# Kernel tuning notes

Measured on AMD Instinct MI355X. Metric: run time of the kernel, lower is better.

The kernel has to match this reference:

```python
import jax, jax.numpy as jnp
import numpy as np

B, S, D, H = 4, 1024, 768, 12
Dh = D // H
EPS = 1e-5


def _layer_norm(x, g, b):
    mu = jnp.mean(x, axis=-1, keepdims=True)
    var = jnp.var(x, axis=-1, keepdims=True)
    return (x - mu) * jax.lax.rsqrt(var + EPS) * g + b


def _mha(q_in, k_in, v_in, Wq, Wk, Wv, Wo, bias):
    # Wq/Wk/Wv: [H, D, Dh] (per-head projections, batched over heads)
    q = jnp.einsum('bsd,hdk->bhsk', q_in, Wq)
    k = jnp.einsum('btd,hdk->bhtk', k_in, Wk)
    v = jnp.einsum('btd,hdk->bhtk', v_in, Wv)
    w = jnp.einsum('bhsk,bhtk->bhst', q, k) * (Dh ** -0.5)
    a = jax.nn.softmax(w + bias, axis=-1)  # bias: 0 / -inf additive mask
    o = jnp.einsum('bhst,bhtk->bhsk', a, v)
    o = o.transpose(0, 2, 1, 3).reshape(q_in.shape[0], q_in.shape[1], H * Dh)  # concat heads
    return o @ Wo


def setup_inputs():
    key = jax.random.key(0)
    ks = jax.random.split(key, 16)
    s = 0.02
    inp = {
        'key_enc': jax.random.normal(ks[0], (B, S, D), jnp.float32),
        'value_enc': jax.random.normal(ks[1], (B, S, D), jnp.float32),
        'x': jax.random.normal(ks[2], (B, S, D), jnp.float32),
        'src_mask': jnp.ones((B, S), jnp.int32),
        'tgt_mask': jnp.ones((B, S), jnp.int32),
        'Wq_m': jax.random.normal(ks[3], (H, D, Dh), jnp.float32) * s,
        'Wk_m': jax.random.normal(ks[4], (H, D, Dh), jnp.float32) * s,
        'Wv_m': jax.random.normal(ks[5], (H, D, Dh), jnp.float32) * s,
        'Wo_m': jax.random.normal(ks[6], (D, D), jnp.float32) * s,
        'Wq_c': jax.random.normal(ks[7], (H, D, Dh), jnp.float32) * s,
        'Wk_c': jax.random.normal(ks[8], (H, D, Dh), jnp.float32) * s,
        'Wv_c': jax.random.normal(ks[9], (H, D, Dh), jnp.float32) * s,
        'Wo_c': jax.random.normal(ks[10], (D, D), jnp.float32) * s,
        'ln1_g': jnp.ones((D,), jnp.float32), 'ln1_b': jnp.zeros((D,), jnp.float32),
        'ln2_g': jnp.ones((D,), jnp.float32), 'ln2_b': jnp.zeros((D,), jnp.float32),
        'ln3_g': jnp.ones((D,), jnp.float32), 'ln3_b': jnp.zeros((D,), jnp.float32),
        'W1': jax.random.normal(ks[11], (D, 4 * D), jnp.float32) * s,
        'b1': jnp.zeros((4 * D,), jnp.float32),
        'W2': jax.random.normal(ks[12], (4 * D, D), jnp.float32) * s,
        'b2': jnp.zeros((D,), jnp.float32),
    }
    return inp


def reference(key_enc, value_enc, x, src_mask, tgt_mask,
              Wq_m, Wk_m, Wv_m, Wo_m, Wq_c, Wk_c, Wv_c, Wo_c,
              ln1_g, ln1_b, ln2_g, ln2_b, ln3_g, ln3_b, W1, b1, W2, b2):
    neg_inf = jnp.float32(-jnp.inf)
    causal = jnp.tril(jnp.ones((S, S), bool))
    # masked self-attn: causal AND target padding mask (mask broadcasts over query rows)
    allow_m = causal[None, None, :, :] & (tgt_mask[:, None, None, :] != 0)
    bias_m = jnp.where(allow_m, jnp.float32(0.0), neg_inf)
    h = _layer_norm(x + _mha(x, x, x, Wq_m, Wk_m, Wv_m, Wo_m, bias_m), ln1_g, ln1_b)
    # cross-attn: keys from `key_enc`, values from `value_enc`, queries from decoder stream
    allow_c = (src_mask[:, None, None, :] != 0)
    bias_c = jnp.where(allow_c, jnp.float32(0.0), neg_inf)
    h = _layer_norm(h + _mha(h, key_enc, value_enc, Wq_c, Wk_c, Wv_c, Wo_c, bias_c), ln2_g, ln2_b)
    # MLP with exact (erf) GELU, as torch nn.GELU default
    mlp = jax.nn.gelu(h @ W1 + b1, approximate=False) @ W2 + b2
    return _layer_norm(h + mlp, ln3_g, ln3_b)
```

## Files before the change

kernel.cpp:

```cpp
#include <hip/hip_runtime.h>
#include <math.h>

#define BB 4
#define SS 1024
#define DD 768
#define HH 12
#define DHD 64
#define MROWS 4096
#define FF 3072
#define WPC (DD * DD)

typedef unsigned short u16;
typedef float f32x4 __attribute__((ext_vector_type(4)));
typedef __bf16 bf16x8 __attribute__((ext_vector_type(8)));
typedef unsigned short u16x8 __attribute__((ext_vector_type(8)));
typedef unsigned short u16x4 __attribute__((ext_vector_type(4)));

static __device__ __forceinline__ float bf2f(u16 u) {
    union { unsigned int i; float f; } c; c.i = ((unsigned int)u) << 16; return c.f;
}
static __device__ __forceinline__ u16 f2bf(float f) {
    return __builtin_bit_cast(u16, static_cast<__bf16>(f));
}
static __device__ __forceinline__ int xcd_swz(int total) {
    const int bid = (int)blockIdx.x;
    return (bid & 7) * (total >> 3) + (bid >> 3);
}

#define LDST 40

static __device__ __forceinline__ void gemm128_core(
    const u16* __restrict__ A, const u16* __restrict__ Bt,
    int K,
    const float* __restrict__ bias, int do_gelu,
    u16* __restrict__ Cbf, int ldcbf, int cboff,
    int row0, int col0, u16* As, u16* Bs)
{
    const int tid  = threadIdx.x;
    const int lane = tid & 63;
    const int w    = tid >> 6;
    const int wm = (w >> 1) * 64;
    const int wn = (w & 1) * 64;

    const int srow = tid >> 1;
    const int skc  = (tid & 1) * 16;

    const u16* Ap = A  + (size_t)(row0 + srow) * K + skc;
    const u16* Bp = Bt + (size_t)(col0 + srow) * K + skc;
    u16* AsW = &As[srow * LDST + skc];
    u16* BsW = &Bs[srow * LDST + skc];

    const int fr = lane & 15;
    const int fk = (lane >> 4) * 8;

    f32x4 acc[4][4] = {};

    u16x8 aa0, aa1, ba0, ba1;
    u16x8 ab0, ab1, bb0, bb1;
    aa0 = *(const u16x8*)(Ap);
    aa1 = *(const u16x8*)(Ap + 8);
    ba0 = *(const u16x8*)(Bp);
    ba1 = *(const u16x8*)(Bp + 8);
    ab0 = *(const u16x8*)(Ap + 32);
    ab1 = *(const u16x8*)(Ap + 40);
    bb0 = *(const u16x8*)(Bp + 32);
    bb1 = *(const u16x8*)(Bp + 40);

    for (int k0 = 0; k0 < K; k0 += 64) {
        if (k0) __syncthreads();
        *(u16x8*)(AsW)     = aa0;
        *(u16x8*)(AsW + 8) = aa1;
        *(u16x8*)(BsW)     = ba0;
        *(u16x8*)(BsW + 8) = ba1;
        __syncthreads();
        if (k0 + 64 < K) {
            aa0 = *(const u16x8*)(Ap + k0 + 64);
            aa1 = *(const u16x8*)(Ap + k0 + 72);
            ba0 = *(const u16x8*)(Bp + k0 + 64);
            ba1 = *(const u16x8*)(Bp + k0 + 72);
        }
        {
            bf16x8 af[4], bfv[4];
#pragma unroll
            for (int mi = 0; mi < 4; ++mi)
                af[mi] = __builtin_bit_cast(bf16x8,
                    *(const u16x8*)(&As[(wm + 16 * mi + fr) * LDST + fk]));
#pragma unroll
            for (int ni = 0; ni < 4; ++ni)
                bfv[ni] = __builtin_bit_cast(bf16x8,
                    *(const u16x8*)(&Bs[(wn + 16 * ni + fr) * LDST + fk]));
#pragma unroll
            for (int mi = 0; mi < 4; ++mi)
#pragma unroll
                for (int ni = 0; ni < 4; ++ni)
                    acc[mi][ni] = __builtin_amdgcn_mfma_f32_16x16x32_bf16(
                        af[mi], bfv[ni], acc[mi][ni], 0, 0, 0);
        }

        __syncthreads();
        *(u16x8*)(AsW)     = ab0;
        *(u16x8*)(AsW + 8) = ab1;
        *(u16x8*)(BsW)     = bb0;
        *(u16x8*)(BsW + 8) = bb1;
        __syncthreads();
        if (k0 + 96 < K) {
            ab0 = *(const u16x8*)(Ap + k0 + 96);
            ab1 = *(const u16x8*)(Ap + k0 + 104);
            bb0 = *(const u16x8*)(Bp + k0 + 96);
            bb1 = *(const u16x8*)(Bp + k0 + 104);
        }
        {
            bf16x8 af[4], bfv[4];
#pragma unroll
            for (int mi = 0; mi < 4; ++mi)
                af[mi] = __builtin_bit_cast(bf16x8,
                    *(const u16x8*)(&As[(wm + 16 * mi + fr) * LDST + fk]));
#pragma unroll
            for (int ni = 0; ni < 4; ++ni)
                bfv[ni] = __builtin_bit_cast(bf16x8,
                    *(const u16x8*)(&Bs[(wn + 16 * ni + fr) * LDST + fk]));
#pragma unroll
            for (int mi = 0; mi < 4; ++mi)
#pragma unroll
                for (int ni = 0; ni < 4; ++ni)
                    acc[mi][ni] = __builtin_amdgcn_mfma_f32_16x16x32_bf16(
                        af[mi], bfv[ni], acc[mi][ni], 0, 0, 0);
        }
    }

    const int orow0 = row0 + wm + (lane >> 4) * 4;
    const int ocol0 = col0 + wn + fr;
#pragma unroll
    for (int mi = 0; mi < 4; ++mi) {
#pragma unroll
        for (int ni = 0; ni < 4; ++ni) {
            const int col = ocol0 + ni * 16;
            const float bv = bias ? bias[col] : 0.0f;
#pragma unroll
            for (int r = 0; r < 4; ++r) {
                const int row = orow0 + mi * 16 + r;
                float v = acc[mi][ni][r] + bv;
                if (do_gelu) v = 0.5f * v * (1.0f + erff(v * 0.70710678118654752f));
                Cbf[(size_t)row * ldcbf + cboff + col] = f2bf(v);
            }
        }
    }
}

__global__ __launch_bounds__(256) void gemm128_mlp1(
    const u16* __restrict__ A, const u16* __restrict__ Bt,
    const float* __restrict__ bias, u16* __restrict__ Cbf)
{
    __shared__ u16 As[128 * LDST];
    __shared__ u16 Bs[128 * LDST];
    const int lid = xcd_swz(24 * 32);
    gemm128_core(A, Bt, DD, bias, 1, Cbf, FF, 0,
                 (lid / 24) * 128, (lid % 24) * 128, As, Bs);
}

__global__ __launch_bounds__(256) void gemm128_proj(
    const u16* __restrict__ BFx, const u16* __restrict__ BFK,
    const u16* __restrict__ BFV, const u16* __restrict__ Wm6,
    u16* __restrict__ QKV, u16* __restrict__ KVc)
{
    __shared__ u16 As[128 * LDST];
    __shared__ u16 Bs[128 * LDST];
    const int fid = xcd_swz(960);
    const u16* A; const u16* B; u16* C; int ldc, coff, row0, col0;
    if (fid < 576) {
        A = BFx; B = Wm6; C = QKV; ldc = 3 * DD; coff = 0;
        row0 = (fid / 18) * 128; col0 = (fid % 18) * 128;
    } else if (fid < 768) {
        const int l = fid - 576;
        A = BFK; B = Wm6 + 4 * WPC; C = KVc; ldc = 2 * DD; coff = 0;
        row0 = (l / 6) * 128; col0 = (l % 6) * 128;
    } else {
        const int l = fid - 768;
        A = BFV; B = Wm6 + 5 * WPC; C = KVc; ldc = 2 * DD; coff = DD;
        row0 = (l / 6) * 128; col0 = (l % 6) * 128;
    }
    gemm128_core(A, B, DD, nullptr, 0, C, ldc, coff, row0, col0, As, Bs);
}

static __device__ __forceinline__ void gemm64_core(
    const u16* __restrict__ A, const u16* __restrict__ Bt,
    int N, int Kstride, int Klen,
    const float* __restrict__ bias,
    const float* __restrict__ residf, const u16* __restrict__ residb,
    u16* __restrict__ Cbf, int ldcbf, int cboff,
    int row0, int col0, u16* As, u16* Bs)
{
    const int tid  = threadIdx.x;
    const int lane = tid & 63;
    const int w    = tid >> 6;
    const int wm = (w >> 1) * 32;
    const int wn = (w & 1) * 64;

    const int arow = tid >> 2;
    const int akc  = (tid & 3) * 8;
    const int brow = tid >> 1;
    const int bkc  = (tid & 1) * 16;

    const u16* Ap = A  + (size_t)(row0 + arow) * Kstride + akc;
    const u16* Bp = Bt + (size_t)(col0 + brow) * Kstride + bkc;
    u16* AsW = &As[arow * LDST + akc];
    u16* BsW = &Bs[brow * LDST + bkc];

    const int fr = lane & 15;
    const int fk = (lane >> 4) * 8;

    f32x4 acc[2][4] = {};

    u16x8 a0, b00, b01, a1, b10, b11;
    a0  = *(const u16x8*)(Ap);
    b00 = *(const u16x8*)(Bp);
    b01 = *(const u16x8*)(Bp + 8);
    a1  = *(const u16x8*)(Ap + 32);
    b10 = *(const u16x8*)(Bp + 32);
    b11 = *(const u16x8*)(Bp + 40);

    for (int k0 = 0; k0 < Klen; k0 += 64) {
        if (k0) __syncthreads();
        *(u16x8*)AsW       = a0;
        *(u16x8*)BsW       = b00;
        *(u16x8*)(BsW + 8) = b01;
        __syncthreads();
        if (k0 + 64 < Klen) {
            a0  = *(const u16x8*)(Ap + k0 + 64);
            b00 = *(const u16x8*)(Bp + k0 + 64);
            b01 = *(const u16x8*)(Bp + k0 + 72);
        }
        {
            bf16x8 af[2], bfv[4];
#pragma unroll
            for (int mi = 0; mi < 2; ++mi)
                af[mi] = __builtin_bit_cast(bf16x8,
                    *(const u16x8*)(&As[(wm + 16 * mi + fr) * LDST + fk]));
#pragma unroll
            for (int ni = 0; ni < 4; ++ni)
                bfv[ni] = __builtin_bit_cast(bf16x8,
                    *(const u16x8*)(&Bs[(wn + 16 * ni + fr) * LDST + fk]));
#pragma unroll
            for (int mi = 0; mi < 2; ++mi)
#pragma unroll
                for (int ni = 0; ni < 4; ++ni)
                    acc[mi][ni] = __builtin_amdgcn_mfma_f32_16x16x32_bf16(
                        af[mi], bfv[ni], acc[mi][ni], 0, 0, 0);
        }

        __syncthreads();
        *(u16x8*)AsW       = a1;
        *(u16x8*)BsW       = b10;
        *(u16x8*)(BsW + 8) = b11;
        __syncthreads();
        if (k0 + 96 < Klen) {
            a1  = *(const u16x8*)(Ap + k0 + 96);
            b10 = *(const u16x8*)(Bp + k0 + 96);
            b11 = *(const u16x8*)(Bp + k0 + 104);
        }
        {
            bf16x8 af[2], bfv[4];
#pragma unroll
            for (int mi = 0; mi < 2; ++mi)
                af[mi] = __builtin_bit_cast(bf16x8,
                    *(const u16x8*)(&As[(wm + 16 * mi + fr) * LDST + fk]));
#pragma unroll
            for (int ni = 0; ni < 4; ++ni)
                bfv[ni] = __builtin_bit_cast(bf16x8,
                    *(const u16x8*)(&Bs[(wn + 16 * ni + fr) * LDST + fk]));
#pragma unroll
            for (int mi = 0; mi < 2; ++mi)
#pragma unroll
                for (int ni = 0; ni < 4; ++ni)
                    acc[mi][ni] = __builtin_amdgcn_mfma_f32_16x16x32_bf16(
                        af[mi], bfv[ni], acc[mi][ni], 0, 0, 0);
        }
    }

    const int orow0 = row0 + wm + (lane >> 4) * 4;
    const int ocol0 = col0 + wn + fr;
#pragma unroll
    for (int mi = 0; mi < 2; ++mi) {
#pragma unroll
        for (int ni = 0; ni < 4; ++ni) {
            const int col = ocol0 + ni * 16;
            const float bv = bias ? bias[col] : 0.0f;
#pragma unroll
            for (int r = 0; r < 4; ++r) {
                const int row = orow0 + mi * 16 + r;
                float v = acc[mi][ni][r] + bv;
                if (residf) v += residf[(size_t)row * N + col];
                if (residb) v += bf2f(residb[(size_t)row * N + col]);
                Cbf[(size_t)row * ldcbf + cboff + col] = f2bf(v);
            }
        }
    }
}

__global__ __launch_bounds__(256) void gemm64(
    const u16* __restrict__ A, const u16* __restrict__ Bt, int K,
    const float* __restrict__ residf, const u16* __restrict__ residb,
    u16* __restrict__ Cbf, int ldcbf)
{
    __shared__ u16 As[64 * LDST];
    __shared__ u16 Bs[128 * LDST];
    const int lid = xcd_swz(6 * 64);
    gemm64_core(A, Bt, DD, K, K, nullptr, residf, residb, Cbf, ldcbf, 0,
                (lid / 6) * 64, (lid % 6) * 128, As, Bs);
}

__global__ __launch_bounds__(256) void gemm64_sk(
    const u16* __restrict__ A, const u16* __restrict__ Bt,
    u16* __restrict__ Cpair)
{
    __shared__ u16 As[64 * LDST];
    __shared__ u16 Bs[128 * LDST];
    const int lid = xcd_swz(6 * 64 * 2);
    const int x = lid % 6;
    const int rem = lid / 6;
    const int y = rem % 64;
    const int z = rem / 64;
    const int koff = z * (FF / 2);
    gemm64_core(A + koff, Bt + koff, DD, FF, FF / 2,
                nullptr, nullptr, nullptr,
                Cpair + (size_t)z * MROWS * DD, DD, 0,
                y * 64, x * 128, As, Bs);
}

static __device__ __forceinline__ void tcvt_body(
    const float* __restrict__ in, u16* __restrict__ out,
    int K, int N, int bx, int by)
{
    __shared__ float t[32][33];
    const int n0 = bx * 32, k0 = by * 32;
    const int tx = threadIdx.x & 31, ty = threadIdx.x >> 5;
#pragma unroll
    for (int j = 0; j < 4; ++j)
        t[ty + j * 8][tx] = in[(size_t)(k0 + ty + j * 8) * N + n0 + tx];
    __syncthreads();
#pragma unroll
    for (int j = 0; j < 4; ++j)
        out[(size_t)(n0 + ty + j * 8) * K + k0 + tx] = f2bf(t[tx][ty + j * 8]);
}

__global__ __launch_bounds__(256) void prep_all(
    const float* __restrict__ x, const float* __restrict__ key_enc,
    const float* __restrict__ value_enc,
    u16* __restrict__ BFx, u16* __restrict__ BFK, u16* __restrict__ BFV,
    const float* __restrict__ wq_m, const float* __restrict__ wk_m,
    const float* __restrict__ wv_m, const float* __restrict__ wq_c,
    const float* __restrict__ wk_c, const float* __restrict__ wv_c,
    u16* __restrict__ Wm6,
    const float* __restrict__ wom, const float* __restrict__ woc,
    const float* __restrict__ w1, const float* __restrict__ w2,
    u16* __restrict__ womt, u16* __restrict__ woct,
    u16* __restrict__ w1t, u16* __restrict__ w2t)
{
    const int fid = (int)blockIdx.x;
    const int tid = threadIdx.x;
    if (fid < 9216) {
        const int z = fid / 3072;
        const float* s = (z == 0) ? x : (z == 1) ? key_enc : value_enc;
        u16* d = (z == 0) ? BFx : (z == 1) ? BFK : BFV;
        const int i = (fid % 3072) * 256 + tid;
        float4 v = ((const float4*)s)[i];
        ushort4 o;
        o.x = f2bf(v.x); o.y = f2bf(v.y); o.z = f2bf(v.z); o.w = f2bf(v.w);
        ((ushort4*)d)[i] = o;
    } else if (fid < 12672) {
        const int l = fid - 9216;
        const int z = l / 48;
        const int r = l % 48;
        const int wi = z / 12, head = z % 12;
        const float* wsel = (wi == 0) ? wq_m : (wi == 1) ? wk_m :
                            (wi == 2) ? wv_m : (wi == 3) ? wq_c :
                            (wi == 4) ? wk_c : wv_c;
        const float* ib = wsel + (size_t)head * DD * DHD;
        u16* ob = Wm6 + (size_t)wi * WPC + (size_t)head * DHD * DD;
        __shared__ float t[32][33];
        const int n0 = (r % 2) * 32, k0 = (r / 2) * 32;
        const int tx = tid & 31, ty = tid >> 5;
#pragma unroll
        for (int j = 0; j < 4; ++j)
            t[ty + j * 8][tx] = ib[(size_t)(k0 + ty + j * 8) * DHD + n0 + tx];
        __syncthreads();
#pragma unroll
        for (int j = 0; j < 4; ++j)
            ob[(size_t)(n0 + ty + j * 8) * DD + k0 + tx] = f2bf(t[tx][ty + j * 8]);
    } else {
        const int l = fid - 12672;
        if (l < 576) {
            tcvt_body(wom, womt, DD, DD, l % 24, l / 24);
        } else if (l < 1152) {
            const int m = l - 576;
            tcvt_body(woc, woct, DD, DD, m % 24, m / 24);
        } else if (l < 3456) {
            const int m = l - 1152;
            tcvt_body(w1, w1t, DD, FF, m % 96, m / 96);
        } else {
            const int m = l - 3456;
            tcvt_body(w2, w2t, FF, DD, m % 24, m / 24);
        }
    }
}

#define KAST 72
#define PAST 136
#define CSC 0.18033688011112042f
__global__ __launch_bounds__(256) void attn_mfma_kernel(
    const u16* __restrict__ Q, int ldq,
    const u16* __restrict__ K, const u16* __restrict__ V, int ldkv,
    const int* __restrict__ kmask, u16* __restrict__ O, int causal)
{
    const int lid = xcd_swz(16 * BB * HH);
    const int qtl = lid % 16;
    const int bh  = lid / 16;
    const int qt = causal ? (15 - qtl) : qtl;
    const int b  = bh / HH;
    const int h  = bh % HH;
    const int tid  = threadIdx.x;
    const int lane = tid & 63;
    const int w    = tid >> 6;
    const int lr = lane & 15;
    const int lg = lane >> 4;

    __shared__ u16 Ks[128 * KAST];
    __shared__ u16 Ps[64 * PAST];
    __shared__ u16 Vt[64 * PAST];

    const int row0 = qt * 64;
    const int q0w  = row0 + w * 16;

    bf16x8 qf[2];
    {
        const u16* qp = Q + (size_t)(b * SS + q0w + lr) * ldq + h * DHD + lg * 8;
        qf[0] = __builtin_bit_cast(bf16x8, *(const u16x8*)(qp));
        qf[1] = __builtin_bit_cast(bf16x8, *(const u16x8*)(qp + 32));
    }

    const int sr  = tid >> 1;
    const int scb = (tid & 1) * 32;
    const int vk  = tid >> 1;
    const int vdb = (tid & 1) * 32;
    const int k6  = vk & 63;
    const int vcol = ((vk >> 6) << 6) | ((k6 & 15) << 2) | (k6 >> 4);

    f32x4 acc[4] = {};
    float lsum[4] = {0.0f, 0.0f, 0.0f, 0.0f};

    const int nkt = causal ? ((qt + 2) >> 1) : 8;

    u16x8 kr0, kr1, kr2, kr3, vr0, vr1, vr2, vr3;
    {
        const u16* kp = K + (size_t)(b * SS + sr) * ldkv + h * DHD + scb;
        kr0 = *(const u16x8*)(kp);
        kr1 = *(const u16x8*)(kp + 8);
        kr2 = *(const u16x8*)(kp + 16);
        kr3 = *(const u16x8*)(kp + 24);
        const u16* vp = V + (size_t)(b * SS + vk) * ldkv + h * DHD + vdb;
        vr0 = *(const u16x8*)(vp);
        vr1 = *(const u16x8*)(vp + 8);
        vr2 = *(const u16x8*)(vp + 16);
        vr3 = *(const u16x8*)(vp + 24);
    }

    for (int kt = 0; kt < nkt; ++kt) {
        const int kcol0 = kt * 128;
        if (kt) __syncthreads();

        *(u16x8*)(&Ks[sr * KAST + scb])      = kr0;
        *(u16x8*)(&Ks[sr * KAST + scb + 8])  = kr1;
        *(u16x8*)(&Ks[sr * KAST + scb + 16]) = kr2;
        *(u16x8*)(&Ks[sr * KAST + scb + 24]) = kr3;
#pragma unroll
        for (int j = 0; j < 8; ++j) Vt[(vdb + j) * PAST + vcol]      = vr0[j];
#pragma unroll
        for (int j = 0; j < 8; ++j) Vt[(vdb + 8 + j) * PAST + vcol]  = vr1[j];
#pragma unroll
        for (int j = 0; j < 8; ++j) Vt[(vdb + 16 + j) * PAST + vcol] = vr2[j];
#pragma unroll
        for (int j = 0; j < 8; ++j) Vt[(vdb + 24 + j) * PAST + vcol] = vr3[j];
        __syncthreads();

        if (kt + 1 < nkt) {
            const int kn = kcol0 + 128;
            const u16* kp = K + (size_t)(b * SS + kn + sr) * ldkv + h * DHD + scb;
            kr0 = *(const u16x8*)(kp);
            kr1 = *(const u16x8*)(kp + 8);
            kr2 = *(const u16x8*)(kp + 16);
            kr3 = *(const u16x8*)(kp + 24);
            const u16* vp = V + (size_t)(b * SS + kn + vk) * ldkv + h * DHD + vdb;
            vr0 = *(const u16x8*)(vp);
            vr1 = *(const u16x8*)(vp + 8);
            vr2 = *(const u16x8*)(vp + 16);
            vr3 = *(const u16x8*)(vp + 24);
        }

        f32x4 s[8] = {};
        __builtin_amdgcn_s_setprio(1);
#pragma unroll
        for (int fi = 0; fi < 8; ++fi) {
            bf16x8 kf0 = __builtin_bit_cast(bf16x8, *(const u16x8*)(&Ks[(fi * 16 + lr) * KAST + lg * 8]));
            bf16x8 kf1 = __builtin_bit_cast(bf16x8, *(const u16x8*)(&Ks[(fi * 16 + lr) * KAST + 32 + lg * 8]));
            s[fi] = __builtin_amdgcn_mfma_f32_16x16x32_bf16(qf[0], kf0, s[fi], 0, 0, 0);
            s[fi] = __builtin_amdgcn_mfma_f32_16x16x32_bf16(qf[1], kf1, s[fi], 0, 0, 0);
        }
        __builtin_amdgcn_s_setprio(0);

        float biasf[8];
#pragma unroll
        for (int fi = 0; fi < 8; ++fi)
            biasf[fi] = kmask[b * SS + kcol0 + fi * 16 + lr] ? 0.0f : -INFINITY;
        const bool diag = (causal != 0) && (kt == nkt - 1);

#pragma unroll
        for (int r = 0; r < 4; ++r) {
            const int qrow = q0w + lg * 4 + r;
            const int prow = (w * 16 + lg * 4 + r) * PAST;
            u16x4 pk0, pk1;
            float rs = 0.0f;
#pragma unroll
            for (int fi = 0; fi < 8; ++fi) {
                float v = fmaf(s[fi][r], CSC, biasf[fi]);
                if (diag) {
                    const int key = kcol0 + fi * 16 + lr;
                    v = (key <= qrow) ? v : -INFINITY;
                }
                const float pv = exp2f(v);
                if (fi < 4) pk0[fi] = f2bf(pv); else pk1[fi - 4] = f2bf(pv);
                rs += pv;
            }
            lsum[r] += rs;
            *(u16x4*)(&Ps[prow + lr * 4])      = pk0;
            *(u16x4*)(&Ps[prow + 64 + lr * 4]) = pk1;
        }

        __builtin_amdgcn_s_setprio(1);
#pragma unroll
        for (int kk = 0; kk < 4; ++kk) {
            bf16x8 pf = __builtin_bit_cast(bf16x8, *(const u16x8*)(&Ps[(w * 16 + lr) * PAST + kk * 32 + lg * 8]));
#pragma unroll
            for (int di = 0; di < 4; ++di) {
                bf16x8 vf = __builtin_bit_cast(bf16x8, *(const u16x8*)(&Vt[(di * 16 + lr) * PAST + kk * 32 + lg * 8]));
                acc[di] = __builtin_amdgcn_mfma_f32_16x16x32_bf16(pf, vf, acc[di], 0, 0, 0);
            }
        }
        __builtin_amdgcn_s_setprio(0);
    }

#pragma unroll
    for (int r = 0; r < 4; ++r) {
        float l = lsum[r];
        l += __shfl_xor(l, 1);
        l += __shfl_xor(l, 2);
        l += __shfl_xor(l, 4);
        l += __shfl_xor(l, 8);
        const float inv = (l > 0.0f) ? (1.0f / l) : 0.0f;
        const size_t orow = (size_t)(b * SS + q0w + lg * 4 + r) * DD + h * DHD;
#pragma unroll
        for (int di = 0; di < 4; ++di)
            O[orow + di * 16 + lr] = f2bf(acc[di][r] * inv);
    }
}

__global__ __launch_bounds__(256) void ln_bf_kernel(
    const u16* __restrict__ X, const float* __restrict__ gma,
    const float* __restrict__ bta, u16* __restrict__ Ybf)
{
    const int row = blockIdx.x;
    const int tid = threadIdx.x;
    const u16* x = X + (size_t)row * DD;

    const float v0 = bf2f(x[tid]);
    const float v1 = bf2f(x[tid + 256]);
    const float v2 = bf2f(x[tid + 512]);

    __shared__ float sd[256];
    sd[tid] = v0 + v1 + v2;
    __syncthreads();
    for (int off = 128; off > 0; off >>= 1) {
        if (tid < off) sd[tid] += sd[tid + off];
        __syncthreads();
    }
    const float mean = sd[0] * (1.0f / 768.0f);
    __syncthreads();

    const float q0 = v0 - mean, q1 = v1 - mean, q2 = v2 - mean;
    sd[tid] = q0 * q0 + q1 * q1 + q2 * q2;
    __syncthreads();
    for (int off = 128; off > 0; off >>= 1) {
        if (tid < off) sd[tid] += sd[tid + off];
        __syncthreads();
    }
    const float var = sd[0] * (1.0f / 768.0f);
    const float inv = rsqrtf(var + 1e-5f);

    u16* yb = Ybf + (size_t)row * DD;
    yb[tid]       = f2bf(q0 * inv * gma[tid]       + bta[tid]);
    yb[tid + 256] = f2bf(q1 * inv * gma[tid + 256] + bta[tid + 256]);
    yb[tid + 512] = f2bf(q2 * inv * gma[tid + 512] + bta[tid + 512]);
}

__global__ __launch_bounds__(256) void ln_red_kernel(
    const u16* __restrict__ P0, const u16* __restrict__ P1,
    const float* __restrict__ bias, const u16* __restrict__ resid,
    const float* __restrict__ gma, const float* __restrict__ bta,
    float* __restrict__ Y)
{
    const int row = blockIdx.x;
    const int tid = threadIdx.x;
    const size_t base = (size_t)row * DD;

    float v[3];
#pragma unroll
    for (int j = 0; j < 3; ++j) {
        const int i = tid + j * 256;
        v[j] = bf2f(P0[base + i]) + bf2f(P1[base + i]) + bias[i] + bf2f(resid[base + i]);
    }

    __shared__ float sd[256];
    sd[tid] = v[0] + v[1] + v[2];
    __syncthreads();
    for (int off = 128; off > 0; off >>= 1) {
        if (tid < off) sd[tid] += sd[tid + off];
        __syncthreads();
    }
    const float mean = sd[0] * (1.0f / 768.0f);
    __syncthreads();

    float q[3];
#pragma unroll
    for (int j = 0; j < 3; ++j) q[j] = v[j] - mean;
    sd[tid] = q[0] * q[0] + q[1] * q[1] + q[2] * q[2];
    __syncthreads();
    for (int off = 128; off > 0; off >>= 1) {
        if (tid < off) sd[tid] += sd[tid + off];
        __syncthreads();
    }
    const float var = sd[0] * (1.0f / 768.0f);
    const float inv = rsqrtf(var + 1e-5f);

    float* y = Y + base;
#pragma unroll
    for (int j = 0; j < 3; ++j) {
        const int i = tid + j * 256;
        y[i] = q[j] * inv * gma[i] + bta[i];
    }
}

extern "C" void kernel_launch(void* const* d_in, const int* in_sizes, int n_in,
                              void* d_out, int out_size, void* d_ws, size_t ws_size,
                              hipStream_t stream)
{
    (void)in_sizes; (void)n_in; (void)out_size; (void)ws_size;

    const float* key_enc   = (const float*)d_in[0];
    const float* value_enc = (const float*)d_in[1];
    const float* x         = (const float*)d_in[2];
    const int*   src_mask  = (const int*)d_in[3];
    const int*   tgt_mask  = (const int*)d_in[4];
    const float* Wq_m = (const float*)d_in[5];
    const float* Wk_m = (const float*)d_in[6];
    const float* Wv_m = (const float*)d_in[7];
    const float* Wo_m = (const float*)d_in[8];
    const float* Wq_c = (const float*)d_in[9];
    const float* Wk_c = (const float*)d_in[10];
    const float* Wv_c = (const float*)d_in[11];
    const float* Wo_c = (const float*)d_in[12];
    const float* ln1_g = (const float*)d_in[13];
    const float* ln1_b = (const float*)d_in[14];
    const float* ln2_g = (const float*)d_in[15];
    const float* ln2_b = (const float*)d_in[16];
    const float* ln3_g = (const float*)d_in[17];
    const float* ln3_b = (const float*)d_in[18];
    const float* W1 = (const float*)d_in[19];
    const float* b1 = (const float*)d_in[20];
    const float* W2 = (const float*)d_in[21];
    const float* b2 = (const float*)d_in[22];

    float* out = (float*)d_out;

    const size_t ACT = (size_t)MROWS * DD;
    char* p = (char*)d_ws;
    u16* QKV  = (u16*)p;   p += 3 * ACT * 2;
    u16* BFx  = (u16*)p;   p += ACT * 2;
    u16* BFK  = (u16*)p;   p += ACT * 2;
    u16* BFV  = (u16*)p;   p += ACT * 2;
    u16* BF1a = (u16*)p;   p += ACT * 2;
    u16* BF1h = (u16*)p;   p += ACT * 2;
    u16* T2bf = (u16*)p;   p += ACT * 2;
    u16* SKKV = (u16*)p;   p += 2 * ACT * 2;
    u16* Wm6  = (u16*)p;   p += 6 * (size_t)WPC * 2;
    u16* Wom_t = (u16*)p;  p += (size_t)WPC * 2;
    u16* Woc_t = (u16*)p;  p += (size_t)WPC * 2;
    u16* W1t  = (u16*)p;   p += (size_t)DD * FF * 2;
    u16* W2t  = (u16*)p;   p += (size_t)DD * FF * 2;
    u16* MID  = QKV;
    u16* KVc  = SKKV;
    u16* SK0  = SKKV;
    u16* SK1  = SKKV + ACT;

    const dim3 blk(256);

    prep_all<<<dim3(18432), blk, 0, stream>>>(
        x, key_enc, value_enc, BFx, BFK, BFV,
        Wq_m, Wk_m, Wv_m, Wq_c, Wk_c, Wv_c, Wm6,
        Wo_m, Wo_c, W1, W2, Wom_t, Woc_t, W1t, W2t);

    gemm128_proj<<<dim3(960), blk, 0, stream>>>(BFx, BFK, BFV, Wm6, QKV, KVc);

    attn_mfma_kernel<<<dim3(768), blk, 0, stream>>>(
        QKV, 3 * DD, QKV + DD, QKV + 2 * DD, 3 * DD, tgt_mask, BF1a, 1);
    gemm64<<<dim3(384), blk, 0, stream>>>(BF1a, Wom_t, DD,
                                          x, nullptr, T2bf, DD);
    ln_bf_kernel<<<MROWS, blk, 0, stream>>>(T2bf, ln1_g, ln1_b, BF1h);

    gemm64<<<dim3(384), blk, 0, stream>>>(BF1h, Wm6 + 3 * WPC, DD,
                                          nullptr, nullptr, QKV, 3 * DD);
    attn_mfma_kernel<<<dim3(768), blk, 0, stream>>>(
        QKV, 3 * DD, KVc, KVc + DD, 2 * DD, src_mask, BF1a, 0);
    gemm64<<<dim3(384), blk, 0, stream>>>(BF1a, Woc_t, DD,
                                          nullptr, BF1h, T2bf, DD);
    ln_bf_kernel<<<MROWS, blk, 0, stream>>>(T2bf, ln2_g, ln2_b, BF1h);

    gemm128_mlp1<<<dim3(768), blk, 0, stream>>>(BF1h, W1t, b1, MID);
    gemm64_sk<<<dim3(768), blk, 0, stream>>>(MID, W2t, SKKV);
    ln_red_kernel<<<MROWS, blk, 0, stream>>>(SK0, SK1, b2, BF1h,
                                             ln3_g, ln3_b, out);
}
```

Baseline: 284.4 us.

## Load GEMM tiles directly into LDS with global_load_lds

Replaces the register-staged global-to-LDS copy in both GEMM cores with direct global_load_lds transfers of 16 bytes per lane. The shared tiles drop the padded stride (40) for a dense 32-wide layout and the K step is halved to 32. The intent is to remove the VGPR round trip and register pressure of the staged copies. In exchange the register prefetch of the next tile is gone, so loads no longer overlap the MFMA work. The unpadded layout may also cause LDS bank conflicts on fragment reads.

After: 282.1 us. About the same (-0.8%).

```diff
diff --git a/kernel.cpp b/kernel.cpp
--- a/kernel.cpp
+++ b/kernel.cpp
@@ -26,8 +26,11 @@
     const int bid = (int)blockIdx.x;
     return (bid & 7) * (total >> 3) + (bid >> 3);
 }
-
-#define LDST 40
+static __device__ __forceinline__ void gload16(const u16* g, u16* l) {
+    __builtin_amdgcn_global_load_lds(
+        (const __attribute__((address_space(1))) void*)g,
+        (__attribute__((address_space(3))) void*)l, 16, 0, 0);
+}
 
 static __device__ __forceinline__ void gemm128_core(
     const u16* __restrict__ A, const u16* __restrict__ Bt,
@@ -42,90 +45,44 @@
     const int wm = (w >> 1) * 64;
     const int wn = (w & 1) * 64;
 
-    const int srow = tid >> 1;
-    const int skc  = (tid & 1) * 16;
-
-    const u16* Ap = A  + (size_t)(row0 + srow) * K + skc;
-    const u16* Bp = Bt + (size_t)(col0 + srow) * K + skc;
-    u16* AsW = &As[srow * LDST + skc];
-    u16* BsW = &Bs[srow * LDST + skc];
+    const int gr = lane >> 2;
+    const int gc = (lane & 3) * 8;
+
+    const u16* Ap = A  + (size_t)(row0 + w * 32 + gr) * K + gc;
+    const u16* Bp = Bt + (size_t)(col0 + w * 32 + gr) * K + gc;
+    u16* AsW = As + (w * 32) * 32;
+    u16* BsW = Bs + (w * 32) * 32;
 
     const int fr = lane & 15;
     const int fk = (lane >> 4) * 8;
+    const u16* ArP = &As[(wm + fr) * 32 + fk];
+    const u16* BrP = &Bs[(wn + fr) * 32 + fk];
 
     f32x4 acc[4][4] = {};
 
-    u16x8 aa0, aa1, ba0, ba1;
-    u16x8 ab0, ab1, bb0, bb1;
-    aa0 = *(const u16x8*)(Ap);
-    aa1 = *(const u16x8*)(Ap + 8);
-    ba0 = *(const u16x8*)(Bp);
-    ba1 = *(const u16x8*)(Bp + 8);
-    ab0 = *(const u16x8*)(Ap + 32);
-    ab1 = *(const u16x8*)(Ap + 40);
-    bb0 = *(const u16x8*)(Bp + 32);
-    bb1 = *(const u16x8*)(Bp + 40);
-
-    for (int k0 = 0; k0 < K; k0 += 64) {
+    for (int k0 = 0; k0 < K; k0 += 32) {
         if (k0) __syncthreads();
-        *(u16x8*)(AsW)     = aa0;
-        *(u16x8*)(AsW + 8) = aa1;
-        *(u16x8*)(BsW)     = ba0;
-        *(u16x8*)(BsW + 8) = ba1;
-        __syncthreads();
-        if (k0 + 64 < K) {
-            aa0 = *(const u16x8*)(Ap + k0 + 64);
-            aa1 = *(const u16x8*)(Ap + k0 + 72);
-            ba0 = *(const u16x8*)(Bp + k0 + 64);
-            ba1 = *(const u16x8*)(Bp + k0 + 72);
-        }
-        {
-            bf16x8 af[4], bfv[4];
-#pragma unroll
-            for (int mi = 0; mi < 4; ++mi)
-                af[mi] = __builtin_bit_cast(bf16x8,
-                    *(const u16x8*)(&As[(wm + 16 * mi + fr) * LDST + fk]));
+        gload16(Ap + k0,          AsW);
+        gload16(Ap + k0 + 16 * K, AsW + 16 * 32);
+        gload16(Bp + k0,          BsW);
+        gload16(Bp + k0 + 16 * K, BsW + 16 * 32);
+        __syncthreads();
+
+        bf16x8 af[4], bfv[4];
+#pragma unroll
+        for (int mi = 0; mi < 4; ++mi)
+            af[mi] = __builtin_bit_cast(bf16x8,
+                *(const u16x8*)(ArP + mi * 16 * 32));
+#pragma unroll
+        for (int ni = 0; ni < 4; ++ni)
+            bfv[ni] = __builtin_bit_cast(bf16x8,
+                *(const u16x8*)(BrP + ni * 16 * 32));
+#pragma unroll
+        for (int mi = 0; mi < 4; ++mi)
 #pragma unroll
             for (int ni = 0; ni < 4; ++ni)
-                bfv[ni] = __builtin_bit_cast(bf16x8,
-                    *(const u16x8*)(&Bs[(wn + 16 * ni + fr) * LDST + fk]));
-#pragma unroll
-            for (int mi = 0; mi < 4; ++mi)
-#pragma unroll
-                for (int ni = 0; ni < 4; ++ni)
-                    acc[mi][ni] = __builtin_amdgcn_mfma_f32_16x16x32_bf16(
-                        af[mi], bfv[ni], acc[mi][ni], 0, 0, 0);
-        }
-
-        __syncthreads();
-        *(u16x8*)(AsW)     = ab0;
-        *(u16x8*)(AsW + 8) = ab1;
-        *(u16x8*)(BsW)     = bb0;
-        *(u16x8*)(BsW + 8) = bb1;
-        __syncthreads();
-        if (k0 + 96 < K) {
-            ab0 = *(const u16x8*)(Ap + k0 + 96);
-            ab1 = *(const u16x8*)(Ap + k0 + 104);
-            bb0 = *(const u16x8*)(Bp + k0 + 96);
-            bb1 = *(const u16x8*)(Bp + k0 + 104);
-        }
-        {
-            bf16x8 af[4], bfv[4];
-#pragma unroll
-            for (int mi = 0; mi < 4; ++mi)
-                af[mi] = __builtin_bit_cast(bf16x8,
-                    *(const u16x8*)(&As[(wm + 16 * mi + fr) * LDST + fk]));
-#pragma unroll
-            for (int ni = 0; ni < 4; ++ni)
-                bfv[ni] = __builtin_bit_cast(bf16x8,
-                    *(const u16x8*)(&Bs[(wn + 16 * ni + fr) * LDST + fk]));
-#pragma unroll
-            for (int mi = 0; mi < 4; ++mi)
-#pragma unroll
-                for (int ni = 0; ni < 4; ++ni)
-                    acc[mi][ni] = __builtin_amdgcn_mfma_f32_16x16x32_bf16(
-                        af[mi], bfv[ni], acc[mi][ni], 0, 0, 0);
-        }
+                acc[mi][ni] = __builtin_amdgcn_mfma_f32_16x16x32_bf16(
+                    af[mi], bfv[ni], acc[mi][ni], 0, 0, 0);
     }
 
     const int orow0 = row0 + wm + (lane >> 4) * 4;
@@ -151,8 +108,8 @@
     const u16* __restrict__ A, const u16* __restrict__ Bt,
     const float* __restrict__ bias, u16* __restrict__ Cbf)
 {
-    __shared__ u16 As[128 * LDST];
-    __shared__ u16 Bs[128 * LDST];
+    __shared__ u16 As[128 * 32];
+    __shared__ u16 Bs[128 * 32];
     const int lid = xcd_swz(24 * 32);
     gemm128_core(A, Bt, DD, bias, 1, Cbf, FF, 0,
                  (lid / 24) * 128, (lid % 24) * 128, As, Bs);
@@ -163,8 +120,8 @@
     const u16* __restrict__ BFV, const u16* __restrict__ Wm6,
     u16* __restrict__ QKV, u16* __restrict__ KVc)
 {
-    __shared__ u16 As[128 * LDST];
-    __shared__ u16 Bs[128 * LDST];
+    __shared__ u16 As[128 * 32];
+    __shared__ u16 Bs[128 * 32];
     const int fid = xcd_swz(960);
     const u16* A; const u16* B; u16* C; int ldc, coff, row0, col0;
     if (fid < 576) {
@@ -196,85 +153,43 @@
     const int wm = (w >> 1) * 32;
     const int wn = (w & 1) * 64;
 
-    const int arow = tid >> 2;
-    const int akc  = (tid & 3) * 8;
-    const int brow = tid >> 1;
-    const int bkc  = (tid & 1) * 16;
-
-    const u16* Ap = A  + (size_t)(row0 + arow) * Kstride + akc;
-    const u16* Bp = Bt + (size_t)(col0 + brow) * Kstride + bkc;
-    u16* AsW = &As[arow * LDST + akc];
-    u16* BsW = &Bs[brow * LDST + bkc];
+    const int gr = lane >> 2;
+    const int gc = (lane & 3) * 8;
+
+    const u16* Ap = A  + (size_t)(row0 + w * 16 + gr) * Kstride + gc;
+    const u16* Bp = Bt + (size_t)(col0 + w * 32 + gr) * Kstride + gc;
+    u16* AsW = As + (w * 16) * 32;
+    u16* BsW = Bs + (w * 32) * 32;
 
     const int fr = lane & 15;
     const int fk = (lane >> 4) * 8;
+    const u16* ArP = &As[(wm + fr) * 32 + fk];
+    const u16* BrP = &Bs[(wn + fr) * 32 + fk];
 
     f32x4 acc[2][4] = {};
 
-    u16x8 a0, b00, b01, a1, b10, b11;
-    a0  = *(const u16x8*)(Ap);
-    b00 = *(const u16x8*)(Bp);
-    b01 = *(const u16x8*)(Bp + 8);
-    a1  = *(const u16x8*)(Ap + 32);
-    b10 = *(const u16x8*)(Bp + 32);
-    b11 = *(const u16x8*)(Bp + 40);
-
-    for (int k0 = 0; k0 < Klen; k0 += 64) {
+    for (int k0 = 0; k0 < Klen; k0 += 32) {
         if (k0) __syncthreads();
-        *(u16x8*)AsW       = a0;
-        *(u16x8*)BsW       = b00;
-        *(u16x8*)(BsW + 8) = b01;
-        __syncthreads();
-        if (k0 + 64 < Klen) {
-            a0  = *(const u16x8*)(Ap + k0 + 64);
-            b00 = *(const u16x8*)(Bp + k0 + 64);
-            b01 = *(const u16x8*)(Bp + k0 + 72);
-        }
-        {
-            bf16x8 af[2], bfv[4];
-#pragma unroll
-            for (int mi = 0; mi < 2; ++mi)
-                af[mi] = __builtin_bit_cast(bf16x8,
-                    *(const u16x8*)(&As[(wm + 16 * mi + fr) * LDST + fk]));
+        gload16(Ap + k0,                AsW);
+        gload16(Bp + k0,                BsW);
+        gload16(Bp + k0 + 16 * Kstride, BsW + 16 * 32);
+        __syncthreads();
+
+        bf16x8 af[2], bfv[4];
+#pragma unroll
+        for (int mi = 0; mi < 2; ++mi)
+            af[mi] = __builtin_bit_cast(bf16x8,
+                *(const u16x8*)(ArP + mi * 16 * 32));
+#pragma unroll
+        for (int ni = 0; ni < 4; ++ni)
+            bfv[ni] = __builtin_bit_cast(bf16x8,
+                *(const u16x8*)(BrP + ni * 16 * 32));
+#pragma unroll
+        for (int mi = 0; mi < 2; ++mi)
 #pragma unroll
             for (int ni = 0; ni < 4; ++ni)
-                bfv[ni] = __builtin_bit_cast(bf16x8,
-                    *(const u16x8*)(&Bs[(wn + 16 * ni + fr) * LDST + fk]));
-#pragma unroll
-            for (int mi = 0; mi < 2; ++mi)
-#pragma unroll
-                for (int ni = 0; ni < 4; ++ni)
-                    acc[mi][ni] = __builtin_amdgcn_mfma_f32_16x16x32_bf16(
-                        af[mi], bfv[ni], acc[mi][ni], 0, 0, 0);
-        }
-
-        __syncthreads();
-        *(u16x8*)AsW       = a1;
-        *(u16x8*)BsW       = b10;
-        *(u16x8*)(BsW + 8) = b11;
-        __syncthreads();
-        if (k0 + 96 < Klen) {
-            a1  = *(const u16x8*)(Ap + k0 + 96);
-            b10 = *(const u16x8*)(Bp + k0 + 96);
-            b11 = *(const u16x8*)(Bp + k0 + 104);
-        }
-        {
-            bf16x8 af[2], bfv[4];
-#pragma unroll
-            for (int mi = 0; mi < 2; ++mi)
-                af[mi] = __builtin_bit_cast(bf16x8,
-                    *(const u16x8*)(&As[(wm + 16 * mi + fr) * LDST + fk]));
-#pragma unroll
-            for (int ni = 0; ni < 4; ++ni)
-                bfv[ni] = __builtin_bit_cast(bf16x8,
-                    *(const u16x8*)(&Bs[(wn + 16 * ni + fr) * LDST + fk]));
-#pragma unroll
-            for (int mi = 0; mi < 2; ++mi)
-#pragma unroll
-                for (int ni = 0; ni < 4; ++ni)
-                    acc[mi][ni] = __builtin_amdgcn_mfma_f32_16x16x32_bf16(
-                        af[mi], bfv[ni], acc[mi][ni], 0, 0, 0);
-        }
+                acc[mi][ni] = __builtin_amdgcn_mfma_f32_16x16x32_bf16(
+                    af[mi], bfv[ni], acc[mi][ni], 0, 0, 0);
     }
 
     const int orow0 = row0 + wm + (lane >> 4) * 4;
@@ -302,8 +217,8 @@
     const float* __restrict__ residf, const u16* __restrict__ residb,
     u16* __restrict__ Cbf, int ldcbf)
 {
-    __shared__ u16 As[64 * LDST];
-    __shared__ u16 Bs[128 * LDST];
+    __shared__ u16 As[64 * 32];
+    __shared__ u16 Bs[128 * 32];
     const int lid = xcd_swz(6 * 64);
     gemm64_core(A, Bt, DD, K, K, nullptr, residf, residb, Cbf, ldcbf, 0,
                 (lid / 6) * 64, (lid % 6) * 128, As, Bs);
@@ -313,8 +228,8 @@
     const u16* __restrict__ A, const u16* __restrict__ Bt,
     u16* __restrict__ Cpair)
 {
-    __shared__ u16 As[64 * LDST];
-    __shared__ u16 Bs[128 * LDST];
+    __shared__ u16 As[64 * 32];
+    __shared__ u16 Bs[128 * 32];
     const int lid = xcd_swz(6 * 64 * 2);
     const int x = lid % 6;
     const int rem = lid / 6;
```
